# Performance work log

Measured on AMD Instinct MI355X. Metric: run time of the kernel, lower is better.

## Reference

```python
import jax, jax.numpy as jnp
import numpy as np

B, HH, WW, C = 16, 64, 64, 256
HEADS, DIM_K, DIM_U, DIM_OUT = 4, 16, 1, 256
DIM_V = DIM_OUT // HEADS  # 64
R = 23
EPS = 1e-3  # keras BatchNormalization default epsilon


def setup_inputs() -> dict:
    key = jax.random.key(0)
    ks = jax.random.split(key, 14)
    def n(i, shape, s=1.0):
        return jax.random.normal(ks[i], shape, dtype=jnp.float32) * s
    def u(i, shape):
        return jax.random.uniform(ks[i], shape, jnp.float32, 0.5, 1.5)
    return {
        "x": n(0, (B, HH, WW, C)),
        "Wq": n(1, (C, DIM_K * HEADS), 0.05),
        "Wk": n(2, (C, DIM_K * DIM_U), 0.05),
        "Wv": n(3, (C, DIM_V * DIM_U), 0.05),
        "gamma_q": u(4, (DIM_K * HEADS,)),
        "beta_q": n(5, (DIM_K * HEADS,), 0.1),
        "mean_q": n(6, (DIM_K * HEADS,), 0.1),
        "var_q": u(7, (DIM_K * HEADS,)),
        "gamma_v": u(8, (DIM_V * DIM_U,)),
        "beta_v": n(9, (DIM_V * DIM_U,), 0.1),
        "mean_v": n(10, (DIM_V * DIM_U,), 0.1),
        "var_v": u(11, (DIM_V * DIM_U,)),
        "pos_w": n(12, (1, R, R, DIM_U, DIM_K), 0.05),  # DHWIO, depth dim = v
        "pos_b": jnp.zeros((DIM_K,), jnp.float32),
    }


def reference(x, Wq, Wk, Wv, gamma_q, beta_q, mean_q, var_q,
              gamma_v, beta_v, mean_v, var_v, pos_w, pos_b):
    b = x.shape[0]
    n_pos = HH * WW
    # 1x1 conv projections = channel matmuls
    q = jnp.einsum('bhwc,cd->bhwd', x, Wq)
    k = jnp.einsum('bhwc,cd->bhwd', x, Wk)
    v = jnp.einsum('bhwc,cd->bhwd', x, Wv)
    # BatchNorm (inference mode: moving stats)
    q = (q - mean_q) * jax.lax.rsqrt(var_q + EPS) * gamma_q + beta_q
    v = (v - mean_v) * jax.lax.rsqrt(var_v + EPS) * gamma_v + beta_v
    # rearranges
    q = q.reshape(b, n_pos, HEADS, DIM_K).transpose(0, 2, 3, 1)    # b h k n
    k = k.reshape(b, n_pos, DIM_U, DIM_K).transpose(0, 2, 3, 1)    # b u k n
    v4 = v.reshape(b, n_pos, DIM_U, DIM_V).transpose(0, 2, 3, 1)   # b u v n
    k = jax.nn.softmax(k, axis=-1)  # softmax over positions
    # content lambda
    Lc = jnp.einsum('bukm,buvm->bkv', k, v4)
    Yc = jnp.einsum('bhkn,bkv->bnhv', q, Lc)
    # positional lambda via local Conv3D over (v, hh, ww) with u channels
    v5 = v4.reshape(b, DIM_U, DIM_V, HH, WW).transpose(0, 2, 3, 4, 1)  # b v hh ww u
    Lp = jax.lax.conv_general_dilated(
        v5, pos_w, window_strides=(1, 1, 1), padding='SAME',
        dimension_numbers=('NDHWC', 'DHWIO', 'NDHWC')) + pos_b         # b v hh ww k
    Lp = Lp.transpose(0, 1, 4, 2, 3).reshape(b, DIM_V, DIM_K, n_pos)   # b v k n
    Yp = jnp.einsum('bhkn,bvkn->bnhv', q, Lp)
    Y = Yc + Yp                                                        # b n h v
    return Y.reshape(b, HH, WW, HEADS * DIM_V)
```

## Files before the change

### kernel.cpp

```cpp
#include <hip/hip_runtime.h>
#include <stdint.h>

typedef __bf16 bf16x8 __attribute__((ext_vector_type(8)));
typedef float  f32x4  __attribute__((ext_vector_type(4)));
typedef float  f32x16 __attribute__((ext_vector_type(16)));
typedef unsigned short u16;

#define WCT_OFF   0u
#define SC_OFF    73728u
#define SH_OFF    74304u
#define BST_OFF   75008u
#define ZB_OFF    524288u
#define MSUM_OFF  640256u
#define LCB_OFF   642304u
#define QP_OFF    707840u
#define KT_OFF    9096448u
#define VT_OFF    11193600u
#define P_OFF     19582208u

__global__ void kP(const float* Wq, const float* Wk, const float* Wv,
                   const float* gq, const float* bq, const float* mq, const float* vq,
                   const float* gv, const float* bv, const float* mv, const float* vvar,
                   const float* pw, char* ws) {
  int t = threadIdx.x;
  int blk = blockIdx.x;
  if (blk < 144) {
    int n = blk, c = t;
    float val;
    if (n < 64)      val = Wq[c * 64 + n];
    else if (n < 80) val = Wk[c * 16 + (n - 64)];
    else             val = Wv[c * 64 + (n - 80)];
    ((__bf16*)(ws + WCT_OFF))[n * 256 + c] = (__bf16)val;
  } else if (blk == 144) {
    if (t < 144) {
      float s, sh;
      if (t < 64)      { s = gq[t] * rsqrtf(vq[t] + 1e-3f); sh = bq[t] - mq[t] * s; }
      else if (t < 80) { s = 1.f; sh = 0.f; }
      else { int i = t - 80; s = gv[i] * rsqrtf(vvar[i] + 1e-3f); sh = bv[i] - mv[i] * s; }
      ((float*)(ws + SC_OFF))[t] = s;
      ((float*)(ws + SH_OFF))[t] = sh;
    }
    f32x4 fz;
    fz[0] = 0.f; fz[1] = 0.f; fz[2] = 0.f; fz[3] = 0.f;
    *(f32x4*)(ws + ZB_OFF + t * 16) = fz;
  } else {
    int dy = blk - 145;
    __bf16* bst = (__bf16*)(ws + BST_OFF) + dy * 8192;
    for (int i = 0; i < 32; ++i) {
      int idx = i * 256 + t;
      int nt = idx >> 10;
      int w2 = (idx >> 9) & 1;
      int l  = (idx >> 3) & 63;
      int e  = idx & 7;
      int n  = nt * 32 + (l & 31);
      int xr = n >> 4, kch = n & 15;
      int o1 = (2 * nt + 5) & ~7;
      int j  = o1 + w2 * 16 + (l >> 5) * 8 + e;
      int dxw = j - xr - 5;
      float val = (dxw >= 0 && dxw < 23) ? pw[(dy * 23 + dxw) * 16 + kch] : 0.f;
      bst[idx] = (__bf16)val;
    }
  }
}

__global__ __launch_bounds__(256) void kA(const float* x, char* ws) {
  __shared__ __align__(16) u16 qlds[64 * 72];
  int t = threadIdx.x, w = t >> 6, l = t & 63;
  int m0 = blockIdx.x * 64;
  int b = m0 >> 12;
  int posb = m0 & 4095;
  const __bf16* wct = (const __bf16*)(ws + WCT_OFF);
  const float* sc = (const float*)(ws + SC_OFF);
  const float* sh = (const float*)(ws + SH_OFF);
  __bf16* qp = (__bf16*)(ws + QP_OFF);
  __bf16* kt = (__bf16*)(ws + KT_OFF);
  __bf16* vt = (__bf16*)(ws + VT_OFF);

  int rl = l & 15;
  int kg = l >> 4;

  f32x4 acc[9];
#pragma unroll
  for (int nf = 0; nf < 9; ++nf)
#pragma unroll
    for (int q = 0; q < 4; ++q) acc[nf][q] = 0.f;

  for (int ks = 0; ks < 8; ++ks) {
    int m = m0 + w * 16 + rl;
    const float* xp = x + (size_t)m * 256 + ks * 32 + kg * 8;
    f32x4 v0 = *(const f32x4*)xp;
    f32x4 v1 = *(const f32x4*)(xp + 4);
    bf16x8 a;
    a[0] = (__bf16)v0[0]; a[1] = (__bf16)v0[1]; a[2] = (__bf16)v0[2]; a[3] = (__bf16)v0[3];
    a[4] = (__bf16)v1[0]; a[5] = (__bf16)v1[1]; a[6] = (__bf16)v1[2]; a[7] = (__bf16)v1[3];
#pragma unroll
    for (int nf = 0; nf < 9; ++nf) {
      bf16x8 bfr = *(const bf16x8*)(wct + (nf * 16 + rl) * 256 + ks * 32 + kg * 8);
      acc[nf] = __builtin_amdgcn_mfma_f32_16x16x32_bf16(a, bfr, acc[nf], 0, 0, 0);
    }
  }

#pragma unroll
  for (int nf = 0; nf < 9; ++nf) {
    int ch = nf * 16 + rl;
    float s = sc[ch], shv = sh[ch];
    int pbase = w * 16 + kg * 4;
    union { __bf16 h[4]; uint2 u; } pk;
#pragma unroll
    for (int r = 0; r < 4; ++r) pk.h[r] = (__bf16)(acc[nf][r] * s + shv);
    if (ch < 64) {
#pragma unroll
      for (int r = 0; r < 4; ++r)
        qlds[(pbase + r) * 72 + ch] = ((u16*)&pk.h[r])[0];
    } else if (ch < 80) {
      *(uint2*)(kt + (size_t)(b * 16 + ch - 64) * 4096 + posb + pbase) = pk.u;
    } else {
      *(uint2*)(vt + (size_t)(b * 64 + ch - 80) * 4096 + posb + pbase) = pk.u;
    }
  }
  __syncthreads();
#pragma unroll
  for (int i = 0; i < 2; ++i) {
    int chunk = t + i * 256;
    int row = chunk >> 3, seg = chunk & 7;
    bf16x8 vq_ = *(const bf16x8*)(qlds + row * 72 + seg * 8);
    *(bf16x8*)(qp + (size_t)(b * 4096 + posb + row) * 64 + seg * 8) = vq_;
  }
}

__global__ void kB1(char* ws) {
  __shared__ float red[256];
  int t = threadIdx.x;
  int b = blockIdx.x >> 4, kk = blockIdx.x & 15;
  const __bf16* kt = (const __bf16*)(ws + KT_OFF) + (size_t)(b * 16 + kk) * 4096;
  __bf16* P = (__bf16*)(ws + P_OFF) + (size_t)(b * 16 + kk) * 4096;
  float v[16];
  bf16x8 c0 = *(const bf16x8*)(kt + t * 16);
  bf16x8 c1 = *(const bf16x8*)(kt + t * 16 + 8);
#pragma unroll
  for (int i = 0; i < 8; ++i) { v[i] = (float)c0[i]; v[8 + i] = (float)c1[i]; }
  float mx = v[0];
#pragma unroll
  for (int i = 1; i < 16; ++i) mx = fmaxf(mx, v[i]);
  red[t] = mx; __syncthreads();
  for (int s = 128; s > 0; s >>= 1) { if (t < s) red[t] = fmaxf(red[t], red[t + s]); __syncthreads(); }
  mx = red[0]; __syncthreads();
  float se = 0.f;
  union { __bf16 h[8]; uint4 u; } p0, p1;
#pragma unroll
  for (int i = 0; i < 8; ++i) { float e = expf(v[i] - mx); se += e; p0.h[i] = (__bf16)e; }
#pragma unroll
  for (int i = 0; i < 8; ++i) { float e = expf(v[8 + i] - mx); se += e; p1.h[i] = (__bf16)e; }
  *(uint4*)(P + t * 16) = p0.u;
  *(uint4*)(P + t * 16 + 8) = p1.u;
  red[t] = se; __syncthreads();
  for (int s = 128; s > 0; s >>= 1) { if (t < s) red[t] += red[t + s]; __syncthreads(); }
  if (t == 0) {
    float* ms = (float*)(ws + MSUM_OFF);
    ms[(b * 16 + kk) * 2] = mx;
    ms[(b * 16 + kk) * 2 + 1] = 1.f / red[0];
  }
}

__global__ __launch_bounds__(256) void kB2(char* ws, const float* pos_b) {
  __shared__ float red[16][256];
  int t = threadIdx.x;
  int b = blockIdx.x >> 6, v = blockIdx.x & 63;
  const __bf16* P = (const __bf16*)(ws + P_OFF) + (size_t)b * 16 * 4096;
  const __bf16* vt = (const __bf16*)(ws + VT_OFF) + (size_t)(b * 64 + v) * 4096;
  const float* ms = (const float*)(ws + MSUM_OFF) + b * 32;
  float acc[16];
#pragma unroll
  for (int i = 0; i < 16; ++i) acc[i] = 0.f;
  for (int c = 0; c < 16; ++c) {
    int p = c * 256 + t;
    float vv = (float)vt[p];
#pragma unroll
    for (int i = 0; i < 16; ++i)
      acc[i] += (float)P[i * 4096 + p] * vv;
  }
#pragma unroll
  for (int i = 0; i < 16; ++i) red[i][t] = acc[i];
  __syncthreads();
  for (int s = 128; s > 0; s >>= 1) {
    if (t < s) {
#pragma unroll
      for (int i = 0; i < 16; ++i) red[i][t] += red[i][t + s];
    }
    __syncthreads();
  }
  if (t < 16) {
    float* lcb = (float*)(ws + LCB_OFF);
    lcb[(b * 16 + t) * 64 + v] = red[t][0] * ms[2 * t + 1] + pos_b[t];
  }
}

__global__ __launch_bounds__(512, 4) void kC(char* ws, float* out) {
  __shared__ __align__(16) u16 img[7][64][64];
  __shared__ __align__(16) u16 qt[2048];
  int t = threadIdx.x, w = t >> 6, l = t & 63;
  int bid = blockIdx.x;
  int swz = (bid & 7) * 256 + (bid >> 3);
  int b = swz >> 7;
  int rest = swz & 127;
  int yp = rest >> 2, xt = rest & 3;
  int y0 = yp * 2, x0g = xt * 16;
  const __bf16* vt  = (const __bf16*)(ws + VT_OFF);
  const __bf16* qp  = (const __bf16*)(ws + QP_OFF);
  const float*  lcb = (const float*)(ws + LCB_OFF) + b * 1024;
  const char*   bstc = (const char*)(ws + BST_OFF);
  const char*   zb   = (const char*)(ws + ZB_OFF) + (t & 255) * 16;

  int yy = w >> 2, ntp = w & 3;
  int hh = l >> 5;
  int o1_8 = ((4 * ntp + 5) & ~7) >> 3;

  int sv = t >> 3, sc8 = t & 7;
  int sgx = x0g - 16 + (sc8 ^ (sv & 7)) * 8;
  bool sokx = (sgx >= 0 && sgx < 64);
  const char* vsrc = (const char*)(vt + (size_t)(b * 64 + sv) * 4096 + sgx);

#define STAGE_IMG(slot, rowv) do {                                             \
    int _r = (rowv);                                                           \
    const char* _s = (sokx && _r >= 0 && _r < 64) ? (vsrc + _r * 128) : zb;    \
    __builtin_amdgcn_global_load_lds(                                          \
      (const __attribute__((address_space(1))) void*)_s,                       \
      (__attribute__((address_space(3))) void*)((char*)&img[0][0][0] + (slot) * 8192 + w * 1024), \
      16, 0, 0);                                                               \
  } while (0)

  STAGE_IMG(0, y0 - 11);
  STAGE_IMG(1, y0 - 10);
  STAGE_IMG(2, y0 - 9);
  STAGE_IMG(3, y0 - 8);
  STAGE_IMG(4, y0 - 7);
  {
    int f0 = t * 4;
    int qyy = f0 >> 10, qx = (f0 >> 6) & 15, qch = f0 & 63;
    *(uint2*)&qt[f0] =
      *(const uint2*)(qp + (size_t)(b * 4096 + (y0 + qyy) * 64 + x0g + qx) * 64 + qch);
  }
  asm volatile("s_waitcnt lgkmcnt(0)" ::: "memory");

  int afoff[2][2];
#pragma unroll
  for (int j = 0; j < 2; ++j)
#pragma unroll
    for (int w2 = 0; w2 < 2; ++w2)
      afoff[j][w2] = ((((2 * ntp + j) * 2 + w2) * 64) + l) * 16;

  f32x16 acc[2][2];
#pragma unroll
  for (int mf = 0; mf < 2; ++mf)
#pragma unroll
    for (int j = 0; j < 2; ++j)
#pragma unroll
      for (int q = 0; q < 16; ++q) acc[mf][j][q] = 0.f;

  int sb = 0;
  for (int i = 0; i < 11; ++i) {
    int dy0 = 2 * i;
    if (i < 10)      asm volatile("s_waitcnt vmcnt(2)" ::: "memory");
    else             asm volatile("s_waitcnt vmcnt(1)" ::: "memory");
    __builtin_amdgcn_s_barrier();
    __builtin_amdgcn_sched_barrier(0);
    asm volatile("" ::: "memory");

    {
      int sA = sb + 5; if (sA >= 7) sA -= 7;
      int sB = sb + 6; if (sB >= 7) sB -= 7;
      if (i <= 9) STAGE_IMG(sA, y0 + dy0 - 6);
      if (i <= 8) STAGE_IMG(sB, y0 + dy0 - 5);
    }

    const char* bdy0 = bstc + dy0 * 16384;
    bf16x8 af0[2][2], af1[2][2], bi0[2][2], bi1[2][2];
#pragma unroll
    for (int j = 0; j < 2; ++j)
#pragma unroll
      for (int w2 = 0; w2 < 2; ++w2) {
        af0[j][w2] = *(const bf16x8*)(bdy0 + afoff[j][w2]);
        af1[j][w2] = *(const bf16x8*)(bdy0 + 16384 + afoff[j][w2]);
      }

    int rA = sb + yy;     if (rA >= 7) rA -= 7;
    int rB = sb + 1 + yy; if (rB >= 7) rB -= 7;
#pragma unroll
    for (int mf = 0; mf < 2; ++mf) {
      int v = mf * 32 + (l & 31);
      int sw = (v & 7);
#pragma unroll
      for (int w2 = 0; w2 < 2; ++w2) {
        int c = ((o1_8 + w2 * 2 + hh) ^ sw) * 8;
        bi0[mf][w2] = *(const bf16x8*)(&img[rA][v][c]);
        bi1[mf][w2] = *(const bf16x8*)(&img[rB][v][c]);
      }
    }
#pragma unroll
    for (int w2 = 0; w2 < 2; ++w2)
#pragma unroll
      for (int j = 0; j < 2; ++j) {
        acc[0][j] = __builtin_amdgcn_mfma_f32_32x32x16_bf16(af0[j][w2], bi0[0][w2], acc[0][j], 0, 0, 0);
        acc[1][j] = __builtin_amdgcn_mfma_f32_32x32x16_bf16(af0[j][w2], bi0[1][w2], acc[1][j], 0, 0, 0);
      }
#pragma unroll
    for (int w2 = 0; w2 < 2; ++w2)
#pragma unroll
      for (int j = 0; j < 2; ++j) {
        acc[0][j] = __builtin_amdgcn_mfma_f32_32x32x16_bf16(af1[j][w2], bi1[0][w2], acc[0][j], 0, 0, 0);
        acc[1][j] = __builtin_amdgcn_mfma_f32_32x32x16_bf16(af1[j][w2], bi1[1][w2], acc[1][j], 0, 0, 0);
      }
    sb += 2; if (sb >= 7) sb -= 7;
  }

  {
    asm volatile("s_waitcnt vmcnt(0)" ::: "memory");
    __builtin_amdgcn_s_barrier();
    __builtin_amdgcn_sched_barrier(0);
    asm volatile("" ::: "memory");
    const char* bdy = bstc + 22 * 16384;
    bf16x8 af[2][2], bi[2][2];
#pragma unroll
    for (int j = 0; j < 2; ++j)
#pragma unroll
      for (int w2 = 0; w2 < 2; ++w2)
        af[j][w2] = *(const bf16x8*)(bdy + afoff[j][w2]);
    int rA = sb + yy; if (rA >= 7) rA -= 7;
#pragma unroll
    for (int mf = 0; mf < 2; ++mf) {
      int v = mf * 32 + (l & 31);
      int sw = (v & 7);
#pragma unroll
      for (int w2 = 0; w2 < 2; ++w2)
        bi[mf][w2] = *(const bf16x8*)(&img[rA][v][((o1_8 + w2 * 2 + hh) ^ sw) * 8]);
    }
#pragma unroll
    for (int w2 = 0; w2 < 2; ++w2)
#pragma unroll
      for (int j = 0; j < 2; ++j) {
        acc[0][j] = __builtin_amdgcn_mfma_f32_32x32x16_bf16(af[j][w2], bi[0][w2], acc[0][j], 0, 0, 0);
        acc[1][j] = __builtin_amdgcn_mfma_f32_32x32x16_bf16(af[j][w2], bi[1][w2], acc[1][j], 0, 0, 0);
      }
  }
#undef STAGE_IMG

  float lc[2][16];
#pragma unroll
  for (int mf = 0; mf < 2; ++mf)
#pragma unroll
    for (int r = 0; r < 16; ++r) {
      int k = (r & 3) + 8 * ((r >> 2) & 1) + 4 * hh;
      lc[mf][r] = lcb[k * 64 + mf * 32 + (l & 31)];
    }
  size_t obase = ((size_t)b * 4096 + (y0 + yy) * 64 + x0g) * 256;
#pragma unroll
  for (int j = 0; j < 2; ++j) {
#pragma unroll
    for (int xh = 0; xh < 2; ++xh) {
      int x_local = 2 * (2 * ntp + j) + xh;
      const u16* qrow = &qt[(yy * 16 + x_local) * 64];
#pragma unroll
      for (int h = 0; h < 4; ++h) {
        float s0 = 0.f, s1 = 0.f;
#pragma unroll
        for (int r8 = 0; r8 < 8; ++r8) {
          int r = xh * 8 + r8;
          int k = (r8 & 3) + 8 * (r8 >> 2) + 4 * hh;
          float qv = (float)(*(const __bf16*)&qrow[h * 16 + k]);
          s0 += qv * (acc[0][j][r] + lc[0][r]);
          s1 += qv * (acc[1][j][r] + lc[1][r]);
        }
        s0 += __shfl_xor(s0, 32);
        s1 += __shfl_xor(s1, 32);
        float val = (l >= 32) ? s1 : s0;
        out[obase + (size_t)x_local * 256 + h * 64 + l] = val;
      }
    }
  }
}

extern "C" void kernel_launch(void* const* d_in, const int* in_sizes, int n_in,
                              void* d_out, int out_size, void* d_ws, size_t ws_size,
                              hipStream_t stream) {
  const float* x   = (const float*)d_in[0];
  const float* Wq  = (const float*)d_in[1];
  const float* Wk  = (const float*)d_in[2];
  const float* Wv  = (const float*)d_in[3];
  const float* gq  = (const float*)d_in[4];
  const float* bq  = (const float*)d_in[5];
  const float* mq  = (const float*)d_in[6];
  const float* vq  = (const float*)d_in[7];
  const float* gv  = (const float*)d_in[8];
  const float* bv  = (const float*)d_in[9];
  const float* mv  = (const float*)d_in[10];
  const float* vvr = (const float*)d_in[11];
  const float* pw  = (const float*)d_in[12];
  const float* pb  = (const float*)d_in[13];
  char* ws = (char*)d_ws;
  float* out = (float*)d_out;

  hipLaunchKernelGGL(kP, dim3(168), dim3(256), 0, stream,
                     Wq, Wk, Wv, gq, bq, mq, vq, gv, bv, mv, vvr, pw, ws);
  hipLaunchKernelGGL(kA, dim3(1024), dim3(256), 0, stream, x, ws);
  hipLaunchKernelGGL(kB1, dim3(256), dim3(256), 0, stream, ws);
  hipLaunchKernelGGL(kB2, dim3(1024), dim3(256), 0, stream, ws, pb);
  hipLaunchKernelGGL(kC, dim3(2048), dim3(512), 0, stream, ws, out);
}
```

Before: 172.6 us.

## Compute content lambda with MFMA tiles instead of scalar dot plus tree reduction

The kB2 kernel that forms the content lambda (softmax(K) times V over positions) now uses bf16 MFMA 16x16x32 instructions. Each block computes a 16x16 (k by v) tile, and the four waves split the position dimension, replacing one block per (b,v) that did scalar FMAs and a 16-wide shared-memory tree reduction. The grid drops from 1024 to 64 blocks, which removes heavy shared-memory reduction and redundant P reads. The cost is low occupancy, since 64 blocks may underfill the GPU.

```diff
diff --git a/kernel.cpp b/kernel.cpp
--- a/kernel.cpp
+++ b/kernel.cpp
@@ -163,36 +163,32 @@
 }
 
 __global__ __launch_bounds__(256) void kB2(char* ws, const float* pos_b) {
-  __shared__ float red[16][256];
-  int t = threadIdx.x;
-  int b = blockIdx.x >> 6, v = blockIdx.x & 63;
-  const __bf16* P = (const __bf16*)(ws + P_OFF) + (size_t)b * 16 * 4096;
-  const __bf16* vt = (const __bf16*)(ws + VT_OFF) + (size_t)(b * 64 + v) * 4096;
+  __shared__ float red[4][16][16];
+  int t = threadIdx.x, w = t >> 6, l = t & 63;
+  int b = blockIdx.x >> 2, vtile = blockIdx.x & 3;
+  const __bf16* P  = (const __bf16*)(ws + P_OFF) + (size_t)b * 16 * 4096;
+  const __bf16* vt = (const __bf16*)(ws + VT_OFF) + (size_t)(b * 64 + vtile * 16) * 4096;
   const float* ms = (const float*)(ws + MSUM_OFF) + b * 32;
-  float acc[16];
-#pragma unroll
-  for (int i = 0; i < 16; ++i) acc[i] = 0.f;
-  for (int c = 0; c < 16; ++c) {
-    int p = c * 256 + t;
-    float vv = (float)vt[p];
-#pragma unroll
-    for (int i = 0; i < 16; ++i)
-      acc[i] += (float)P[i * 4096 + p] * vv;
-  }
-#pragma unroll
-  for (int i = 0; i < 16; ++i) red[i][t] = acc[i];
+  int ar = l & 15;
+  int kg = l >> 4;
+  const __bf16* pA = P  + (size_t)ar * 4096 + w * 1024 + kg * 8;
+  const __bf16* pB = vt + (size_t)ar * 4096 + w * 1024 + kg * 8;
+  f32x4 acc;
+  acc[0] = 0.f; acc[1] = 0.f; acc[2] = 0.f; acc[3] = 0.f;
+#pragma unroll 4
+  for (int ks = 0; ks < 32; ++ks) {
+    bf16x8 a  = *(const bf16x8*)(pA + ks * 32);
+    bf16x8 bb = *(const bf16x8*)(pB + ks * 32);
+    acc = __builtin_amdgcn_mfma_f32_16x16x32_bf16(a, bb, acc, 0, 0, 0);
+  }
+#pragma unroll
+  for (int r = 0; r < 4; ++r)
+    red[w][kg * 4 + r][ar] = acc[r];
   __syncthreads();
-  for (int s = 128; s > 0; s >>= 1) {
-    if (t < s) {
-#pragma unroll
-      for (int i = 0; i < 16; ++i) red[i][t] += red[i][t + s];
-    }
-    __syncthreads();
-  }
-  if (t < 16) {
-    float* lcb = (float*)(ws + LCB_OFF);
-    lcb[(b * 16 + t) * 64 + v] = red[t][0] * ms[2 * t + 1] + pos_b[t];
-  }
+  int k = t >> 4, v = t & 15;
+  float s = red[0][k][v] + red[1][k][v] + red[2][k][v] + red[3][k][v];
+  ((float*)(ws + LCB_OFF))[(b * 16 + k) * 64 + vtile * 16 + v] =
+      s * ms[2 * k + 1] + pos_b[k];
 }
 
 __global__ __launch_bounds__(512, 4) void kC(char* ws, float* out) {
@@ -403,6 +399,6 @@
                      Wq, Wk, Wv, gq, bq, mq, vq, gv, bv, mv, vvr, pw, ws);
   hipLaunchKernelGGL(kA, dim3(1024), dim3(256), 0, stream, x, ws);
   hipLaunchKernelGGL(kB1, dim3(256), dim3(256), 0, stream, ws);
-  hipLaunchKernelGGL(kB2, dim3(1024), dim3(256), 0, stream, ws, pb);
+  hipLaunchKernelGGL(kB2, dim3(64), dim3(256), 0, stream, ws, pb);
   hipLaunchKernelGGL(kC, dim3(2048), dim3(512), 0, stream, ws, out);
 }
```

Result: faster. 168.2 us (-2.5%).
